# Performance work log

Measured on AMD Instinct MI355X. Metric: run time of the kernel, lower is better.

Reference implementation:

```python
import jax, jax.numpy as jnp
import numpy as np


def setup_inputs() -> dict:
    key = jax.random.key(0)
    k1, k2, k3, k4 = jax.random.split(key, 4)
    B, S, E, H = 8, 2048, 1024, 64
    x = jax.random.normal(k1, (B, S, E), dtype=jnp.float32)
    scale = 1.0 / np.sqrt(E)
    Wq = jax.random.normal(k2, (E, H), dtype=jnp.float32) * scale
    Wk = jax.random.normal(k3, (E, H), dtype=jnp.float32) * scale
    Wv = jax.random.normal(k4, (E, H), dtype=jnp.float32) * scale
    return {"x": x, "Wq": Wq, "Wk": Wk, "Wv": Wv}


def reference(x, Wq, Wk, Wv):
    # x: [B, S, E]; Wq/Wk/Wv: [E, H]
    B, S, E = x.shape
    H = Wq.shape[1]
    q = x @ Wq  # [B, S, H]
    k = x @ Wk
    v = x @ Wv
    inv_sqrt_h = 1.0 / jnp.sqrt(jnp.asarray(H, dtype=x.dtype))
    att = jnp.einsum("bqh,bkh->bqk", q, k) * inv_sqrt_h  # [B, S, S]
    causal = jnp.tril(jnp.ones((S, S), dtype=bool))
    att = jnp.where(causal, att, jnp.asarray(-jnp.inf, dtype=att.dtype))
    att = jax.nn.softmax(att, axis=-1)
    # dropout p=0.0 (eval) -> identity
    return jnp.einsum("bqk,bkh->bqh", att, v)  # [B, S, H]
```

## Files before the change

### kernel.cpp

```cpp
#include <hip/hip_runtime.h>
#include <math.h>

typedef __attribute__((ext_vector_type(8))) short bf16x8;
typedef __attribute__((ext_vector_type(16))) float fx16;

#define SEQ 2048
#define HD 64

__device__ __forceinline__ unsigned f2bf_bits(float f){
  unsigned u = __float_as_uint(f);
  return (u + 0x7fffu + ((u >> 16) & 1u)) >> 16;
}
__device__ __forceinline__ unsigned cvt_pk_bf16(float a, float b){
  unsigned r;
  asm("v_cvt_pk_bf16_f32 %0, %1, %2" : "=v"(r) : "v"(a), "v"(b));
  return r;
}
__device__ __forceinline__ float lo16f(unsigned u){ return __uint_as_float(u << 16); }
__device__ __forceinline__ float hi16f(unsigned u){ return __uint_as_float(u & 0xffff0000u); }
union U8 { bf16x8 v; short s[8]; unsigned u[4]; };

__device__ __forceinline__ fx16 mfma_bf16(bf16x8 a, bf16x8 b, fx16 c){
  return __builtin_amdgcn_mfma_f32_32x32x16_bf16(a, b, c, 0, 0, 0);
}
__device__ __forceinline__ fx16 fzero(){
  fx16 z;
#pragma unroll
  for (int i = 0; i < 16; ++i) z[i] = 0.f;
  return z;
}

__global__ __launch_bounds__(256) void wconv_kernel(
    const float* __restrict__ Wq, const float* __restrict__ Wk, const float* __restrict__ Wv,
    short* __restrict__ wsB)
{
  int gid = blockIdx.x * 4 + (threadIdx.x >> 6);
  int lane = threadIdx.x & 63;
  int l31 = lane & 31, h = lane >> 5;
  int half = gid & 1;
  int rem = gid >> 1;
  int t = rem % 6;
  int stage = rem / 6;
  int n = t * 32 + l31;
  int mat = n >> 6, col = n & 63;
  const float* W = (mat == 0) ? Wq : (mat == 1) ? Wk : Wv;
  int kbase = stage * 16 + h * 8;
  U8 o;
#pragma unroll
  for (int i = 0; i < 8; ++i) {
    float f = W[(size_t)(kbase + i) * 64 + col];
    unsigned hb = f2bf_bits(f);
    if (half == 0) o.s[i] = (short)hb;
    else {
      float hf = __uint_as_float(hb << 16);
      o.s[i] = (short)f2bf_bits(f - hf);
    }
  }
  *(bf16x8*)(wsB + (size_t)gid * 512 + lane * 8) = o.v;
}

__global__ __launch_bounds__(512) void proj_kernel(
    const float* __restrict__ x, const short* __restrict__ wsB,
    short* __restrict__ qh, short* __restrict__ ql,
    short* __restrict__ kh, short* __restrict__ kl,
    short* __restrict__ vth, short* __restrict__ vtl)
{
  __shared__ float Rx[4][3 * 16 * 64];
  __shared__ float Vb[32 * 68];

  const int tid = threadIdx.x;
  const int lane = tid & 63, w = tid >> 6;
  const int l31 = lane & 31, h = lane >> 5;
  const int ksel = w >> 1;
  const int nsel = w & 1;
  const int row0 = blockIdx.x * 32;
  const size_t xbase = (size_t)(row0 + l31) * 1024;

  fx16 acc[3];
#pragma unroll
  for (int t = 0; t < 3; ++t) acc[t] = fzero();

#pragma unroll 4
  for (int s = 0; s < 16; ++s) {
    const int stage = ksel * 16 + s;
    const int k = stage * 16 + h * 8;
    float4 fa = *(const float4*)(x + xbase + k);
    float4 fb = *(const float4*)(x + xbase + k + 4);
    U8 ah, al;
    ah.u[0] = cvt_pk_bf16(fa.x, fa.y);
    ah.u[1] = cvt_pk_bf16(fa.z, fa.w);
    ah.u[2] = cvt_pk_bf16(fb.x, fb.y);
    ah.u[3] = cvt_pk_bf16(fb.z, fb.w);
    al.u[0] = cvt_pk_bf16(fa.x - lo16f(ah.u[0]), fa.y - hi16f(ah.u[0]));
    al.u[1] = cvt_pk_bf16(fa.z - lo16f(ah.u[1]), fa.w - hi16f(ah.u[1]));
    al.u[2] = cvt_pk_bf16(fb.x - lo16f(ah.u[2]), fb.y - hi16f(ah.u[2]));
    al.u[3] = cvt_pk_bf16(fb.z - lo16f(ah.u[3]), fb.w - hi16f(ah.u[3]));
#pragma unroll
    for (int tt = 0; tt < 3; ++tt) {
      const int tg = nsel * 3 + tt;
      const size_t g2 = ((size_t)stage * 6 + tg) * 2;
      bf16x8 Bh = *(const bf16x8*)(wsB + g2 * 512 + lane * 8);
      bf16x8 Bl = *(const bf16x8*)(wsB + g2 * 512 + 512 + lane * 8);
      acc[tt] = mfma_bf16(al.v, Bh, acc[tt]);
      acc[tt] = mfma_bf16(ah.v, Bl, acc[tt]);
      acc[tt] = mfma_bf16(ah.v, Bh, acc[tt]);
    }
  }

  if (ksel == 1 || ksel == 3) {
    const int ws_ = (ksel == 1) ? nsel : 2 + nsel;
#pragma unroll
    for (int t = 0; t < 3; ++t)
#pragma unroll
      for (int r = 0; r < 16; ++r)
        Rx[ws_][t * 1024 + r * 64 + lane] = acc[t][r];
  }
  __syncthreads();
  if (ksel == 0 || ksel == 2) {
    const int rs_ = (ksel == 0) ? nsel : 2 + nsel;
#pragma unroll
    for (int t = 0; t < 3; ++t)
#pragma unroll
      for (int r = 0; r < 16; ++r)
        acc[t][r] += Rx[rs_][t * 1024 + r * 64 + lane];
  }
  __syncthreads();
  if (ksel == 2) {
#pragma unroll
    for (int t = 0; t < 3; ++t)
#pragma unroll
      for (int r = 0; r < 16; ++r)
        Rx[nsel][t * 1024 + r * 64 + lane] = acc[t][r];
  }
  __syncthreads();
  if (ksel == 0) {
#pragma unroll
    for (int t = 0; t < 3; ++t) {
      const int tg = nsel * 3 + t;
      const int mat = tg >> 1;
      const int colb = (tg & 1) * 32 + l31;
#pragma unroll
      for (int r = 0; r < 16; ++r)
        acc[t][r] += Rx[nsel][t * 1024 + r * 64 + lane];
      if (mat < 2) {
        short* dh = (mat == 0) ? qh : kh;
        short* dl = (mat == 0) ? ql : kl;
#pragma unroll
        for (int r = 0; r < 16; ++r) {
          float f = acc[t][r];
          int rowg = row0 + (r & 3) + 8 * (r >> 2) + 4 * h;
          unsigned hb = f2bf_bits(f);
          float hf = __uint_as_float(hb << 16);
          unsigned lb = f2bf_bits(f - hf);
          dh[(size_t)rowg * 64 + colb] = (short)hb;
          dl[(size_t)rowg * 64 + colb] = (short)lb;
        }
      } else {
#pragma unroll
        for (int r = 0; r < 16; ++r) {
          float f = acc[t][r];
          int srel = (r & 3) + 8 * (r >> 2) + 4 * h;
          Vb[srel * 68 + (tg - 4) * 32 + l31] = f;
        }
      }
    }
  }
  __syncthreads();
  if (tid < 256) {
    int d = tid >> 2, s8 = (tid & 3) * 8;
    int bb = row0 >> 11, s0 = row0 & 2047;
    U8 hv, lv;
#pragma unroll
    for (int ss = 0; ss < 8; ++ss) {
      float f = Vb[(s8 + ss) * 68 + d];
      unsigned hb = f2bf_bits(f);
      float hf = __uint_as_float(hb << 16);
      hv.s[ss] = (short)hb;
      lv.s[ss] = (short)f2bf_bits(f - hf);
    }
    size_t o = (size_t)(bb * 64 + d) * 2048 + s0 + s8;
    *(bf16x8*)(vth + o) = hv.v;
    *(bf16x8*)(vtl + o) = lv.v;
  }
}

__global__ __launch_bounds__(64) void attn_kernel(
    const short* __restrict__ qh, const short* __restrict__ ql,
    const short* __restrict__ kh, const short* __restrict__ kl,
    const short* __restrict__ vth, const short* __restrict__ vtl,
    float* __restrict__ segO, float* __restrict__ segL, float* __restrict__ segM)
{
  const int bid = blockIdx.x;
  const int b = bid & 7;
  int r = bid >> 3;
  int qt = 0, acc = 0;
  while (r >= acc + ((qt + 5) / 5)) { acc += (qt + 5) / 5; ++qt; }
  const int sg = r - acc;
  const int nk = qt + 1;
  const int kt0 = sg * 5;
  int nsteps = nk - kt0; if (nsteps > 5) nsteps = 5;

  const int lane = threadIdx.x;
  const int l31 = lane & 31, h = lane >> 5;
  const int qabs = qt * 32 + l31;

  bf16x8 qf0[4], qf1[4];
  {
    size_t qrow = ((size_t)b * 2048 + qabs) * 64;
#pragma unroll
    for (int ds = 0; ds < 4; ++ds) {
      qf0[ds] = *(const bf16x8*)(qh + qrow + ds * 16 + 8 * h);
      qf1[ds] = *(const bf16x8*)(ql + qrow + ds * 16 + 8 * h);
    }
  }

  fx16 acc0 = fzero(), acc1 = fzero();
  float Mrun = -3e38f, lrun = 0.f;

  for (int it = 0; it < nsteps; ++it) {
    const int kt = kt0 + it;
    bf16x8 kah[4], kal[4];
    {
      const size_t koff = ((size_t)b * 2048 + (size_t)kt * 32 + l31) * 64 + 8 * h;
#pragma unroll
      for (int ds = 0; ds < 4; ++ds) {
        kah[ds] = *(const bf16x8*)(kh + koff + ds * 16);
        kal[ds] = *(const bf16x8*)(kl + koff + ds * 16);
      }
    }
    bf16x8 vfh[2][2], vfl[2][2];
#pragma unroll
    for (int kp = 0; kp < 2; ++kp)
#pragma unroll
      for (int md = 0; md < 2; ++md) {
        const size_t vrow = (size_t)(b * 64 + md * 32 + l31) * 2048 + kt * 32 + kp * 16 + 8 * h;
        vfh[kp][md] = *(const bf16x8*)(vth + vrow);
        vfl[kp][md] = *(const bf16x8*)(vtl + vrow);
      }

    fx16 stA = fzero(), stB = fzero();
    __builtin_amdgcn_s_setprio(1);
#pragma unroll
    for (int ds = 0; ds < 4; ++ds) {
      stA = mfma_bf16(kah[ds], qf0[ds], stA);
      stB = mfma_bf16(kal[ds], qf0[ds], stB);
      stB = mfma_bf16(kah[ds], qf1[ds], stB);
    }
    __builtin_amdgcn_s_setprio(0);

    float sv[16];
    const bool diag = (kt == qt);
#pragma unroll
    for (int r2 = 0; r2 < 16; ++r2) {
      float s = (stA[r2] + stB[r2]) * 0.125f;
      if (diag) {
        int ka = kt * 32 + (r2 & 3) + 8 * (r2 >> 2) + 4 * h;
        if (ka > qabs) s = -3e38f;
      }
      sv[r2] = s;
    }
    float tm = sv[0];
#pragma unroll
    for (int r2 = 1; r2 < 16; ++r2) tm = fmaxf(tm, sv[r2]);
    tm = fmaxf(tm, __shfl_xor(tm, 32, 64));
    float Mnew = fmaxf(Mrun, tm);
    float alpha = __expf(Mrun - Mnew);
    Mrun = Mnew;
    float psum = 0.f;
#pragma unroll
    for (int r2 = 0; r2 < 16; ++r2) { sv[r2] = __expf(sv[r2] - Mnew); psum += sv[r2]; }
    psum += __shfl_xor(psum, 32, 64);
    lrun = lrun * alpha + psum;
#pragma unroll
    for (int r2 = 0; r2 < 16; ++r2) { acc0[r2] *= alpha; acc1[r2] *= alpha; }

    unsigned chv[8], clv[8];
#pragma unroll
    for (int q2 = 0; q2 < 8; ++q2) {
      unsigned c = cvt_pk_bf16(sv[2 * q2], sv[2 * q2 + 1]);
      chv[q2] = c;
      clv[q2] = cvt_pk_bf16(sv[2 * q2] - lo16f(c), sv[2 * q2 + 1] - hi16f(c));
    }
#pragma unroll
    for (int kp = 0; kp < 2; ++kp) {
      U8 ph, pl;
      {
        unsigned c0 = chv[4 * kp], c1 = chv[4 * kp + 1], c2 = chv[4 * kp + 2], c3 = chv[4 * kp + 3];
        unsigned x0 = (unsigned)__shfl_xor((int)c0, 32, 64);
        unsigned x1 = (unsigned)__shfl_xor((int)c1, 32, 64);
        unsigned x2 = (unsigned)__shfl_xor((int)c2, 32, 64);
        unsigned x3 = (unsigned)__shfl_xor((int)c3, 32, 64);
        ph.u[0] = h ? x2 : c0;  ph.u[1] = h ? x3 : c1;
        ph.u[2] = h ? c2 : x0;  ph.u[3] = h ? c3 : x1;
        c0 = clv[4 * kp]; c1 = clv[4 * kp + 1]; c2 = clv[4 * kp + 2]; c3 = clv[4 * kp + 3];
        x0 = (unsigned)__shfl_xor((int)c0, 32, 64);
        x1 = (unsigned)__shfl_xor((int)c1, 32, 64);
        x2 = (unsigned)__shfl_xor((int)c2, 32, 64);
        x3 = (unsigned)__shfl_xor((int)c3, 32, 64);
        pl.u[0] = h ? x2 : c0;  pl.u[1] = h ? x3 : c1;
        pl.u[2] = h ? c2 : x0;  pl.u[3] = h ? c3 : x1;
      }
      __builtin_amdgcn_s_setprio(1);
      acc0 = mfma_bf16(vfl[kp][0], ph.v, acc0);
      acc0 = mfma_bf16(vfh[kp][0], pl.v, acc0);
      acc0 = mfma_bf16(vfh[kp][0], ph.v, acc0);
      acc1 = mfma_bf16(vfl[kp][1], ph.v, acc1);
      acc1 = mfma_bf16(vfh[kp][1], pl.v, acc1);
      acc1 = mfma_bf16(vfh[kp][1], ph.v, acc1);
      __builtin_amdgcn_s_setprio(0);
    }
  }

  float* o = segO + (size_t)bid * 2048;
#pragma unroll
  for (int md = 0; md < 2; ++md) {
#pragma unroll
    for (int r2 = 0; r2 < 16; ++r2) {
      int d = md * 32 + (r2 & 3) + 8 * (r2 >> 2) + 4 * h;
      float val = md ? acc1[r2] : acc0[r2];
      o[d * 32 + l31] = val;
    }
  }
  if (h == 0) {
    segL[(size_t)bid * 32 + l31] = lrun;
    segM[(size_t)bid * 32 + l31] = Mrun;
  }
}

__global__ __launch_bounds__(256) void combine_kernel(
    const float* __restrict__ segO, const float* __restrict__ segL,
    const float* __restrict__ segM, float* __restrict__ out)
{
  __shared__ float Sc[13][32];
  __shared__ float Linv[32];
  __shared__ float Ot[64 * 40];

  const int bq = blockIdx.x;
  const int b = bq >> 6, qt = bq & 63;
  const int nsg = (qt + 5) / 5;
  int base = 0;
  for (int i = 0; i < qt; ++i) base += (i + 5) / 5;
  const int tid = threadIdx.x;

  if (tid < 32) {
    float M = -3e38f;
    for (int s = 0; s < nsg; ++s)
      M = fmaxf(M, segM[(size_t)((base + s) * 8 + b) * 32 + tid]);
    float L = 0.f;
    for (int s = 0; s < nsg; ++s) {
      float e = __expf(segM[(size_t)((base + s) * 8 + b) * 32 + tid] - M);
      Sc[s][tid] = e;
      L += e * segL[(size_t)((base + s) * 8 + b) * 32 + tid];
    }
    Linv[tid] = 1.f / L;
  }
  __syncthreads();
  {
#pragma unroll
    for (int i = tid; i < 512; i += 256) {
      int d = i >> 3, q4 = (i & 7) * 4;
      float4 a = {0.f, 0.f, 0.f, 0.f};
      for (int s = 0; s < nsg; ++s) {
        float4 v = *(const float4*)(segO + (size_t)((base + s) * 8 + b) * 2048 + d * 32 + q4);
        a.x += Sc[s][q4 + 0] * v.x;
        a.y += Sc[s][q4 + 1] * v.y;
        a.z += Sc[s][q4 + 2] * v.z;
        a.w += Sc[s][q4 + 3] * v.w;
      }
      *(float4*)&Ot[d * 40 + q4] = a;
    }
  }
  __syncthreads();
  {
    const int q = tid >> 3, dc = (tid & 7) * 8;
    const float inv = Linv[q];
    float* dst = out + ((size_t)b * 2048 + qt * 32 + q) * 64 + dc;
#pragma unroll
    for (int i = 0; i < 2; ++i) {
      float4 o;
      o.x = Ot[(dc + 4 * i + 0) * 40 + q] * inv;
      o.y = Ot[(dc + 4 * i + 1) * 40 + q] * inv;
      o.z = Ot[(dc + 4 * i + 2) * 40 + q] * inv;
      o.w = Ot[(dc + 4 * i + 3) * 40 + q] * inv;
      *(float4*)(dst + 4 * i) = o;
    }
  }
}

extern "C" void kernel_launch(void* const* d_in, const int* in_sizes, int n_in,
                              void* d_out, int out_size, void* d_ws, size_t ws_size,
                              hipStream_t stream) {
  const float* x  = (const float*)d_in[0];
  const float* Wq = (const float*)d_in[1];
  const float* Wk = (const float*)d_in[2];
  const float* Wv = (const float*)d_in[3];

  char* wsb = (char*)d_ws;
  short* wsB = (short*)(wsb + 0);
  short* qh  = (short*)(wsb + 786432);
  short* ql  = (short*)(wsb + 2883584);
  short* kh  = (short*)(wsb + 4980736);
  short* kl  = (short*)(wsb + 7077888);
  short* vth = (short*)(wsb + 9175040);
  short* vtl = (short*)(wsb + 11272192);
  float* segO = (float*)(wsb + 13369344);
  float* segL = (float*)(wsb + 42336256);
  float* segM = (float*)(wsb + 42788864);

  wconv_kernel<<<192, 256, 0, stream>>>(Wq, Wk, Wv, wsB);
  proj_kernel<<<512, 512, 0, stream>>>(x, wsB, qh, ql, kh, kl, vth, vtl);
  attn_kernel<<<3536, 64, 0, stream>>>(qh, ql, kh, kl, vth, vtl, segO, segL, segM);
  combine_kernel<<<512, 256, 0, stream>>>(segO, segL, segM, (float*)d_out);
}
```

Measured before the change: 102.9 us.

## Double row tiles in projection and attention to reuse weight and K/V fragments

The projection kernel now handles 64 rows per block instead of 32, so each weight fragment load feeds two MFMA row tiles. The cross-wave K-split reduction becomes a serial accumulate into a smaller shared buffer. The attention kernel processes two 32-row query groups per wave, sharing each loaded K/V tile between them, and the segment and combine layouts change to match. This halves global loads of weights and K/V per unit of work, at the cost of higher register pressure, fewer blocks (less parallelism), and more serial reduction barriers in projection.

```diff
diff --git a/kernel.cpp b/kernel.cpp
--- a/kernel.cpp
+++ b/kernel.cpp
@@ -65,122 +65,235 @@
     short* __restrict__ kh, short* __restrict__ kl,
     short* __restrict__ vth, short* __restrict__ vtl)
 {
-  __shared__ float Rx[4][3 * 16 * 64];
-  __shared__ float Vb[32 * 68];
+  __shared__ float Rx[2][6144];
 
   const int tid = threadIdx.x;
   const int lane = tid & 63, w = tid >> 6;
   const int l31 = lane & 31, h = lane >> 5;
   const int ksel = w >> 1;
   const int nsel = w & 1;
-  const int row0 = blockIdx.x * 32;
-  const size_t xbase = (size_t)(row0 + l31) * 1024;
-
-  fx16 acc[3];
-#pragma unroll
-  for (int t = 0; t < 3; ++t) acc[t] = fzero();
-
-#pragma unroll 4
+  const int row0 = blockIdx.x * 64;
+  const size_t xb0 = (size_t)(row0 + l31) * 1024;
+  const size_t xb1 = (size_t)(row0 + 32 + l31) * 1024;
+
+  fx16 a0[3], a1[3];
+#pragma unroll
+  for (int t = 0; t < 3; ++t) { a0[t] = fzero(); a1[t] = fzero(); }
+
+#pragma unroll 2
   for (int s = 0; s < 16; ++s) {
     const int stage = ksel * 16 + s;
     const int k = stage * 16 + h * 8;
-    float4 fa = *(const float4*)(x + xbase + k);
-    float4 fb = *(const float4*)(x + xbase + k + 4);
-    U8 ah, al;
-    ah.u[0] = cvt_pk_bf16(fa.x, fa.y);
-    ah.u[1] = cvt_pk_bf16(fa.z, fa.w);
-    ah.u[2] = cvt_pk_bf16(fb.x, fb.y);
-    ah.u[3] = cvt_pk_bf16(fb.z, fb.w);
-    al.u[0] = cvt_pk_bf16(fa.x - lo16f(ah.u[0]), fa.y - hi16f(ah.u[0]));
-    al.u[1] = cvt_pk_bf16(fa.z - lo16f(ah.u[1]), fa.w - hi16f(ah.u[1]));
-    al.u[2] = cvt_pk_bf16(fb.x - lo16f(ah.u[2]), fb.y - hi16f(ah.u[2]));
-    al.u[3] = cvt_pk_bf16(fb.z - lo16f(ah.u[3]), fb.w - hi16f(ah.u[3]));
+    float4 fa0 = *(const float4*)(x + xb0 + k);
+    float4 fb0 = *(const float4*)(x + xb0 + k + 4);
+    float4 fa1 = *(const float4*)(x + xb1 + k);
+    float4 fb1 = *(const float4*)(x + xb1 + k + 4);
+    U8 ah0, al0, ah1, al1;
+    ah0.u[0] = cvt_pk_bf16(fa0.x, fa0.y);
+    ah0.u[1] = cvt_pk_bf16(fa0.z, fa0.w);
+    ah0.u[2] = cvt_pk_bf16(fb0.x, fb0.y);
+    ah0.u[3] = cvt_pk_bf16(fb0.z, fb0.w);
+    al0.u[0] = cvt_pk_bf16(fa0.x - lo16f(ah0.u[0]), fa0.y - hi16f(ah0.u[0]));
+    al0.u[1] = cvt_pk_bf16(fa0.z - lo16f(ah0.u[1]), fa0.w - hi16f(ah0.u[1]));
+    al0.u[2] = cvt_pk_bf16(fb0.x - lo16f(ah0.u[2]), fb0.y - hi16f(ah0.u[2]));
+    al0.u[3] = cvt_pk_bf16(fb0.z - lo16f(ah0.u[3]), fb0.w - hi16f(ah0.u[3]));
+    ah1.u[0] = cvt_pk_bf16(fa1.x, fa1.y);
+    ah1.u[1] = cvt_pk_bf16(fa1.z, fa1.w);
+    ah1.u[2] = cvt_pk_bf16(fb1.x, fb1.y);
+    ah1.u[3] = cvt_pk_bf16(fb1.z, fb1.w);
+    al1.u[0] = cvt_pk_bf16(fa1.x - lo16f(ah1.u[0]), fa1.y - hi16f(ah1.u[0]));
+    al1.u[1] = cvt_pk_bf16(fa1.z - lo16f(ah1.u[1]), fa1.w - hi16f(ah1.u[1]));
+    al1.u[2] = cvt_pk_bf16(fb1.x - lo16f(ah1.u[2]), fb1.y - hi16f(ah1.u[2]));
+    al1.u[3] = cvt_pk_bf16(fb1.z - lo16f(ah1.u[3]), fb1.w - hi16f(ah1.u[3]));
 #pragma unroll
     for (int tt = 0; tt < 3; ++tt) {
       const int tg = nsel * 3 + tt;
       const size_t g2 = ((size_t)stage * 6 + tg) * 2;
       bf16x8 Bh = *(const bf16x8*)(wsB + g2 * 512 + lane * 8);
       bf16x8 Bl = *(const bf16x8*)(wsB + g2 * 512 + 512 + lane * 8);
-      acc[tt] = mfma_bf16(al.v, Bh, acc[tt]);
-      acc[tt] = mfma_bf16(ah.v, Bl, acc[tt]);
-      acc[tt] = mfma_bf16(ah.v, Bh, acc[tt]);
-    }
-  }
-
-  if (ksel == 1 || ksel == 3) {
-    const int ws_ = (ksel == 1) ? nsel : 2 + nsel;
-#pragma unroll
-    for (int t = 0; t < 3; ++t)
-#pragma unroll
-      for (int r = 0; r < 16; ++r)
-        Rx[ws_][t * 1024 + r * 64 + lane] = acc[t][r];
-  }
-  __syncthreads();
-  if (ksel == 0 || ksel == 2) {
-    const int rs_ = (ksel == 0) ? nsel : 2 + nsel;
-#pragma unroll
-    for (int t = 0; t < 3; ++t)
-#pragma unroll
-      for (int r = 0; r < 16; ++r)
-        acc[t][r] += Rx[rs_][t * 1024 + r * 64 + lane];
+      a0[tt] = mfma_bf16(al0.v, Bh, a0[tt]);
+      a0[tt] = mfma_bf16(ah0.v, Bl, a0[tt]);
+      a0[tt] = mfma_bf16(ah0.v, Bh, a0[tt]);
+      a1[tt] = mfma_bf16(al1.v, Bh, a1[tt]);
+      a1[tt] = mfma_bf16(ah1.v, Bl, a1[tt]);
+      a1[tt] = mfma_bf16(ah1.v, Bh, a1[tt]);
+    }
+  }
+
+  float* slot = &Rx[nsel][0];
+  __syncthreads();
+  if (ksel == 3) {
+#pragma unroll
+    for (int tt = 0; tt < 3; ++tt)
+#pragma unroll
+      for (int r = 0; r < 16; ++r) {
+        slot[((tt * 2 + 0) * 16 + r) * 64 + lane] = a0[tt][r];
+        slot[((tt * 2 + 1) * 16 + r) * 64 + lane] = a1[tt][r];
+      }
   }
   __syncthreads();
   if (ksel == 2) {
 #pragma unroll
-    for (int t = 0; t < 3; ++t)
-#pragma unroll
-      for (int r = 0; r < 16; ++r)
-        Rx[nsel][t * 1024 + r * 64 + lane] = acc[t][r];
+    for (int tt = 0; tt < 3; ++tt)
+#pragma unroll
+      for (int r = 0; r < 16; ++r) {
+        slot[((tt * 2 + 0) * 16 + r) * 64 + lane] += a0[tt][r];
+        slot[((tt * 2 + 1) * 16 + r) * 64 + lane] += a1[tt][r];
+      }
+  }
+  __syncthreads();
+  if (ksel == 1) {
+#pragma unroll
+    for (int tt = 0; tt < 3; ++tt)
+#pragma unroll
+      for (int r = 0; r < 16; ++r) {
+        slot[((tt * 2 + 0) * 16 + r) * 64 + lane] += a0[tt][r];
+        slot[((tt * 2 + 1) * 16 + r) * 64 + lane] += a1[tt][r];
+      }
   }
   __syncthreads();
   if (ksel == 0) {
 #pragma unroll
-    for (int t = 0; t < 3; ++t) {
-      const int tg = nsel * 3 + t;
+    for (int tt = 0; tt < 3; ++tt)
+#pragma unroll
+      for (int r = 0; r < 16; ++r) {
+        a0[tt][r] += slot[((tt * 2 + 0) * 16 + r) * 64 + lane];
+        a1[tt][r] += slot[((tt * 2 + 1) * 16 + r) * 64 + lane];
+      }
+  }
+  __syncthreads();
+
+  float* Vb = &Rx[0][0];
+  if (ksel == 0) {
+#pragma unroll
+    for (int tt = 0; tt < 3; ++tt) {
+      const int tg = nsel * 3 + tt;
       const int mat = tg >> 1;
       const int colb = (tg & 1) * 32 + l31;
-#pragma unroll
-      for (int r = 0; r < 16; ++r)
-        acc[t][r] += Rx[nsel][t * 1024 + r * 64 + lane];
       if (mat < 2) {
         short* dh = (mat == 0) ? qh : kh;
         short* dl = (mat == 0) ? ql : kl;
 #pragma unroll
-        for (int r = 0; r < 16; ++r) {
-          float f = acc[t][r];
-          int rowg = row0 + (r & 3) + 8 * (r >> 2) + 4 * h;
-          unsigned hb = f2bf_bits(f);
-          float hf = __uint_as_float(hb << 16);
-          unsigned lb = f2bf_bits(f - hf);
-          dh[(size_t)rowg * 64 + colb] = (short)hb;
-          dl[(size_t)rowg * 64 + colb] = (short)lb;
-        }
+        for (int m = 0; m < 2; ++m)
+#pragma unroll
+          for (int r = 0; r < 16; ++r) {
+            float f = (m ? a1[tt][r] : a0[tt][r]);
+            int rowg = row0 + m * 32 + (r & 3) + 8 * (r >> 2) + 4 * h;
+            unsigned hb = f2bf_bits(f);
+            float hf = __uint_as_float(hb << 16);
+            unsigned lb = f2bf_bits(f - hf);
+            dh[(size_t)rowg * 64 + colb] = (short)hb;
+            dl[(size_t)rowg * 64 + colb] = (short)lb;
+          }
       } else {
 #pragma unroll
-        for (int r = 0; r < 16; ++r) {
-          float f = acc[t][r];
-          int srel = (r & 3) + 8 * (r >> 2) + 4 * h;
-          Vb[srel * 68 + (tg - 4) * 32 + l31] = f;
-        }
+        for (int m = 0; m < 2; ++m)
+#pragma unroll
+          for (int r = 0; r < 16; ++r) {
+            float f = (m ? a1[tt][r] : a0[tt][r]);
+            int srel = m * 32 + (r & 3) + 8 * (r >> 2) + 4 * h;
+            Vb[srel * 68 + (tg - 4) * 32 + l31] = f;
+          }
       }
     }
   }
   __syncthreads();
   if (tid < 256) {
-    int d = tid >> 2, s8 = (tid & 3) * 8;
+    int d = tid >> 2, sc = (tid & 3) * 16;
     int bb = row0 >> 11, s0 = row0 & 2047;
-    U8 hv, lv;
-#pragma unroll
-    for (int ss = 0; ss < 8; ++ss) {
-      float f = Vb[(s8 + ss) * 68 + d];
+    U8 hv0, hv1, lv0, lv1;
+#pragma unroll
+    for (int ss = 0; ss < 16; ++ss) {
+      float f = Vb[(sc + ss) * 68 + d];
       unsigned hb = f2bf_bits(f);
       float hf = __uint_as_float(hb << 16);
-      hv.s[ss] = (short)hb;
-      lv.s[ss] = (short)f2bf_bits(f - hf);
-    }
-    size_t o = (size_t)(bb * 64 + d) * 2048 + s0 + s8;
-    *(bf16x8*)(vth + o) = hv.v;
-    *(bf16x8*)(vtl + o) = lv.v;
+      unsigned lb = f2bf_bits(f - hf);
+      if (ss < 8) { hv0.s[ss] = (short)hb; lv0.s[ss] = (short)lb; }
+      else        { hv1.s[ss - 8] = (short)hb; lv1.s[ss - 8] = (short)lb; }
+    }
+    size_t o = (size_t)(bb * 64 + d) * 2048 + s0 + sc;
+    *(bf16x8*)(vth + o) = hv0.v;  *(bf16x8*)(vth + o + 8) = hv1.v;
+    *(bf16x8*)(vtl + o) = lv0.v;  *(bf16x8*)(vtl + o + 8) = lv1.v;
+  }
+}
+
+__device__ __forceinline__ void attn_step_qg(
+    const bf16x8* __restrict__ qh_, const bf16x8* __restrict__ ql_,
+    const bf16x8* __restrict__ kah, const bf16x8* __restrict__ kal,
+    const bf16x8 (*vfh)[2], const bf16x8 (*vfl)[2],
+    fx16& accA, fx16& accB, float& Mrun, float& lrun,
+    const int kt, const int qt, const int qg, const int h, const int qabs)
+{
+  fx16 st = fzero();
+  __builtin_amdgcn_s_setprio(1);
+#pragma unroll
+  for (int ds = 0; ds < 4; ++ds) {
+    st = mfma_bf16(kah[ds], qh_[ds], st);
+    st = mfma_bf16(kal[ds], qh_[ds], st);
+    st = mfma_bf16(kah[ds], ql_[ds], st);
+  }
+  __builtin_amdgcn_s_setprio(0);
+
+  float sv[16];
+  const bool diag = (kt == 2 * qt + qg);
+#pragma unroll
+  for (int r2 = 0; r2 < 16; ++r2) {
+    float s = st[r2] * 0.125f;
+    if (diag) {
+      int ka = kt * 32 + (r2 & 3) + 8 * (r2 >> 2) + 4 * h;
+      if (ka > qabs) s = -3e38f;
+    }
+    sv[r2] = s;
+  }
+  float tm = sv[0];
+#pragma unroll
+  for (int r2 = 1; r2 < 16; ++r2) tm = fmaxf(tm, sv[r2]);
+  tm = fmaxf(tm, __shfl_xor(tm, 32, 64));
+  float Mnew = fmaxf(Mrun, tm);
+  float alpha = __expf(Mrun - Mnew);
+  Mrun = Mnew;
+  float psum = 0.f;
+#pragma unroll
+  for (int r2 = 0; r2 < 16; ++r2) { sv[r2] = __expf(sv[r2] - Mnew); psum += sv[r2]; }
+  psum += __shfl_xor(psum, 32, 64);
+  lrun = lrun * alpha + psum;
+#pragma unroll
+  for (int r2 = 0; r2 < 16; ++r2) { accA[r2] *= alpha; accB[r2] *= alpha; }
+
+  unsigned chv[8], clv[8];
+#pragma unroll
+  for (int q2 = 0; q2 < 8; ++q2) {
+    unsigned c = cvt_pk_bf16(sv[2 * q2], sv[2 * q2 + 1]);
+    chv[q2] = c;
+    clv[q2] = cvt_pk_bf16(sv[2 * q2] - lo16f(c), sv[2 * q2 + 1] - hi16f(c));
+  }
+#pragma unroll
+  for (int kp = 0; kp < 2; ++kp) {
+    U8 ph, pl;
+    {
+      unsigned c0 = chv[4 * kp], c1 = chv[4 * kp + 1], c2 = chv[4 * kp + 2], c3 = chv[4 * kp + 3];
+      unsigned x0 = (unsigned)__shfl_xor((int)c0, 32, 64);
+      unsigned x1 = (unsigned)__shfl_xor((int)c1, 32, 64);
+      unsigned x2 = (unsigned)__shfl_xor((int)c2, 32, 64);
+      unsigned x3 = (unsigned)__shfl_xor((int)c3, 32, 64);
+      ph.u[0] = h ? x2 : c0;  ph.u[1] = h ? x3 : c1;
+      ph.u[2] = h ? c2 : x0;  ph.u[3] = h ? c3 : x1;
+      c0 = clv[4 * kp]; c1 = clv[4 * kp + 1]; c2 = clv[4 * kp + 2]; c3 = clv[4 * kp + 3];
+      x0 = (unsigned)__shfl_xor((int)c0, 32, 64);
+      x1 = (unsigned)__shfl_xor((int)c1, 32, 64);
+      x2 = (unsigned)__shfl_xor((int)c2, 32, 64);
+      x3 = (unsigned)__shfl_xor((int)c3, 32, 64);
+      pl.u[0] = h ? x2 : c0;  pl.u[1] = h ? x3 : c1;
+      pl.u[2] = h ? c2 : x0;  pl.u[3] = h ? c3 : x1;
+    }
+    __builtin_amdgcn_s_setprio(1);
+    accA = mfma_bf16(vfl[kp][0], ph.v, accA);
+    accA = mfma_bf16(vfh[kp][0], pl.v, accA);
+    accA = mfma_bf16(vfh[kp][0], ph.v, accA);
+    accB = mfma_bf16(vfl[kp][1], ph.v, accB);
+    accB = mfma_bf16(vfh[kp][1], pl.v, accB);
+    accB = mfma_bf16(vfh[kp][1], ph.v, accB);
+    __builtin_amdgcn_s_setprio(0);
   }
 }
 
@@ -194,28 +307,32 @@
   const int b = bid & 7;
   int r = bid >> 3;
   int qt = 0, acc = 0;
-  while (r >= acc + ((qt + 5) / 5)) { acc += (qt + 5) / 5; ++qt; }
+  while (r >= acc + ((2 * qt + 6) / 5)) { acc += (2 * qt + 6) / 5; ++qt; }
   const int sg = r - acc;
-  const int nk = qt + 1;
+  const int nk = 2 * qt + 2;
   const int kt0 = sg * 5;
   int nsteps = nk - kt0; if (nsteps > 5) nsteps = 5;
 
   const int lane = threadIdx.x;
   const int l31 = lane & 31, h = lane >> 5;
-  const int qabs = qt * 32 + l31;
-
-  bf16x8 qf0[4], qf1[4];
+  const int qa0 = qt * 64 + l31;
+  const int qa1 = qt * 64 + 32 + l31;
+
+  bf16x8 q0h[4], q0l[4], q1h[4], q1l[4];
   {
-    size_t qrow = ((size_t)b * 2048 + qabs) * 64;
+    size_t r0 = ((size_t)b * 2048 + qt * 64 + l31) * 64 + 8 * h;
+    size_t r1 = r0 + 32 * 64;
 #pragma unroll
     for (int ds = 0; ds < 4; ++ds) {
-      qf0[ds] = *(const bf16x8*)(qh + qrow + ds * 16 + 8 * h);
-      qf1[ds] = *(const bf16x8*)(ql + qrow + ds * 16 + 8 * h);
-    }
-  }
-
-  fx16 acc0 = fzero(), acc1 = fzero();
-  float Mrun = -3e38f, lrun = 0.f;
+      q0h[ds] = *(const bf16x8*)(qh + r0 + ds * 16);
+      q0l[ds] = *(const bf16x8*)(ql + r0 + ds * 16);
+      q1h[ds] = *(const bf16x8*)(qh + r1 + ds * 16);
+      q1l[ds] = *(const bf16x8*)(ql + r1 + ds * 16);
+    }
+  }
+
+  fx16 a00 = fzero(), a01 = fzero(), a10 = fzero(), a11 = fzero();
+  float M0 = -3e38f, L0 = 0.f, M1 = -3e38f, L1 = 0.f;
 
   for (int it = 0; it < nsteps; ++it) {
     const int kt = kt0 + it;
@@ -238,92 +355,25 @@
         vfl[kp][md] = *(const bf16x8*)(vtl + vrow);
       }
 
-    fx16 stA = fzero(), stB = fzero();
-    __builtin_amdgcn_s_setprio(1);
-#pragma unroll
-    for (int ds = 0; ds < 4; ++ds) {
-      stA = mfma_bf16(kah[ds], qf0[ds], stA);
-      stB = mfma_bf16(kal[ds], qf0[ds], stB);
-      stB = mfma_bf16(kah[ds], qf1[ds], stB);
-    }
-    __builtin_amdgcn_s_setprio(0);
-
-    float sv[16];
-    const bool diag = (kt == qt);
-#pragma unroll
-    for (int r2 = 0; r2 < 16; ++r2) {
-      float s = (stA[r2] + stB[r2]) * 0.125f;
-      if (diag) {
-        int ka = kt * 32 + (r2 & 3) + 8 * (r2 >> 2) + 4 * h;
-        if (ka > qabs) s = -3e38f;
-      }
-      sv[r2] = s;
-    }
-    float tm = sv[0];
-#pragma unroll
-    for (int r2 = 1; r2 < 16; ++r2) tm = fmaxf(tm, sv[r2]);
-    tm = fmaxf(tm, __shfl_xor(tm, 32, 64));
-    float Mnew = fmaxf(Mrun, tm);
-    float alpha = __expf(Mrun - Mnew);
-    Mrun = Mnew;
-    float psum = 0.f;
-#pragma unroll
-    for (int r2 = 0; r2 < 16; ++r2) { sv[r2] = __expf(sv[r2] - Mnew); psum += sv[r2]; }
-    psum += __shfl_xor(psum, 32, 64);
-    lrun = lrun * alpha + psum;
-#pragma unroll
-    for (int r2 = 0; r2 < 16; ++r2) { acc0[r2] *= alpha; acc1[r2] *= alpha; }
-
-    unsigned chv[8], clv[8];
-#pragma unroll
-    for (int q2 = 0; q2 < 8; ++q2) {
-      unsigned c = cvt_pk_bf16(sv[2 * q2], sv[2 * q2 + 1]);
-      chv[q2] = c;
-      clv[q2] = cvt_pk_bf16(sv[2 * q2] - lo16f(c), sv[2 * q2 + 1] - hi16f(c));
-    }
-#pragma unroll
-    for (int kp = 0; kp < 2; ++kp) {
-      U8 ph, pl;
-      {
-        unsigned c0 = chv[4 * kp], c1 = chv[4 * kp + 1], c2 = chv[4 * kp + 2], c3 = chv[4 * kp + 3];
-        unsigned x0 = (unsigned)__shfl_xor((int)c0, 32, 64);
-        unsigned x1 = (unsigned)__shfl_xor((int)c1, 32, 64);
-        unsigned x2 = (unsigned)__shfl_xor((int)c2, 32, 64);
-        unsigned x3 = (unsigned)__shfl_xor((int)c3, 32, 64);
-        ph.u[0] = h ? x2 : c0;  ph.u[1] = h ? x3 : c1;
-        ph.u[2] = h ? c2 : x0;  ph.u[3] = h ? c3 : x1;
-        c0 = clv[4 * kp]; c1 = clv[4 * kp + 1]; c2 = clv[4 * kp + 2]; c3 = clv[4 * kp + 3];
-        x0 = (unsigned)__shfl_xor((int)c0, 32, 64);
-        x1 = (unsigned)__shfl_xor((int)c1, 32, 64);
-        x2 = (unsigned)__shfl_xor((int)c2, 32, 64);
-        x3 = (unsigned)__shfl_xor((int)c3, 32, 64);
-        pl.u[0] = h ? x2 : c0;  pl.u[1] = h ? x3 : c1;
-        pl.u[2] = h ? c2 : x0;  pl.u[3] = h ? c3 : x1;
-      }
-      __builtin_amdgcn_s_setprio(1);
-      acc0 = mfma_bf16(vfl[kp][0], ph.v, acc0);
-      acc0 = mfma_bf16(vfh[kp][0], pl.v, acc0);
-      acc0 = mfma_bf16(vfh[kp][0], ph.v, acc0);
-      acc1 = mfma_bf16(vfl[kp][1], ph.v, acc1);
-      acc1 = mfma_bf16(vfh[kp][1], pl.v, acc1);
-      acc1 = mfma_bf16(vfh[kp][1], ph.v, acc1);
-      __builtin_amdgcn_s_setprio(0);
-    }
-  }
-
-  float* o = segO + (size_t)bid * 2048;
-#pragma unroll
-  for (int md = 0; md < 2; ++md) {
-#pragma unroll
-    for (int r2 = 0; r2 < 16; ++r2) {
-      int d = md * 32 + (r2 & 3) + 8 * (r2 >> 2) + 4 * h;
-      float val = md ? acc1[r2] : acc0[r2];
-      o[d * 32 + l31] = val;
-    }
+    if (kt <= 2 * qt)
+      attn_step_qg(q0h, q0l, kah, kal, vfh, vfl, a00, a01, M0, L0, kt, qt, 0, h, qa0);
+    attn_step_qg(q1h, q1l, kah, kal, vfh, vfl, a10, a11, M1, L1, kt, qt, 1, h, qa1);
+  }
+
+  float* o = segO + (size_t)bid * 4096;
+#pragma unroll
+  for (int r2 = 0; r2 < 16; ++r2) {
+    int d0 = (r2 & 3) + 8 * (r2 >> 2) + 4 * h;
+    o[d0 * 64 + l31]             = a00[r2];
+    o[(32 + d0) * 64 + l31]      = a01[r2];
+    o[d0 * 64 + 32 + l31]        = a10[r2];
+    o[(32 + d0) * 64 + 32 + l31] = a11[r2];
   }
   if (h == 0) {
-    segL[(size_t)bid * 32 + l31] = lrun;
-    segM[(size_t)bid * 32 + l31] = Mrun;
+    segL[(size_t)bid * 64 + l31]      = L0;
+    segL[(size_t)bid * 64 + 32 + l31] = L1;
+    segM[(size_t)bid * 64 + l31]      = M0;
+    segM[(size_t)bid * 64 + 32 + l31] = M1;
   }
 }
 
@@ -331,57 +381,56 @@
     const float* __restrict__ segO, const float* __restrict__ segL,
     const float* __restrict__ segM, float* __restrict__ out)
 {
-  __shared__ float Sc[13][32];
-  __shared__ float Linv[32];
-  __shared__ float Ot[64 * 40];
+  __shared__ float Sc[13][64];
+  __shared__ float Linv[64];
+  __shared__ float Ot[64 * 68];
 
   const int bq = blockIdx.x;
-  const int b = bq >> 6, qt = bq & 63;
-  const int nsg = (qt + 5) / 5;
+  const int b = bq >> 5, qt = bq & 31;
+  const int nsg = (2 * qt + 6) / 5;
   int base = 0;
-  for (int i = 0; i < qt; ++i) base += (i + 5) / 5;
+  for (int i = 0; i < qt; ++i) base += (2 * i + 6) / 5;
   const int tid = threadIdx.x;
 
-  if (tid < 32) {
+  if (tid < 64) {
     float M = -3e38f;
     for (int s = 0; s < nsg; ++s)
-      M = fmaxf(M, segM[(size_t)((base + s) * 8 + b) * 32 + tid]);
+      M = fmaxf(M, segM[(size_t)((base + s) * 8 + b) * 64 + tid]);
     float L = 0.f;
     for (int s = 0; s < nsg; ++s) {
-      float e = __expf(segM[(size_t)((base + s) * 8 + b) * 32 + tid] - M);
+      float e = __expf(segM[(size_t)((base + s) * 8 + b) * 64 + tid] - M);
       Sc[s][tid] = e;
-      L += e * segL[(size_t)((base + s) * 8 + b) * 32 + tid];
+      L += e * segL[(size_t)((base + s) * 8 + b) * 64 + tid];
     }
     Linv[tid] = 1.f / L;
   }
   __syncthreads();
   {
-#pragma unroll
-    for (int i = tid; i < 512; i += 256) {
-      int d = i >> 3, q4 = (i & 7) * 4;
+    for (int i = tid; i < 1024; i += 256) {
+      int d = i >> 4, q4 = (i & 15) * 4;
       float4 a = {0.f, 0.f, 0.f, 0.f};
       for (int s = 0; s < nsg; ++s) {
-        float4 v = *(const float4*)(segO + (size_t)((base + s) * 8 + b) * 2048 + d * 32 + q4);
+        float4 v = *(const float4*)(segO + (size_t)((base + s) * 8 + b) * 4096 + d * 64 + q4);
         a.x += Sc[s][q4 + 0] * v.x;
         a.y += Sc[s][q4 + 1] * v.y;
         a.z += Sc[s][q4 + 2] * v.z;
         a.w += Sc[s][q4 + 3] * v.w;
       }
-      *(float4*)&Ot[d * 40 + q4] = a;
+      *(float4*)&Ot[d * 68 + q4] = a;
     }
   }
   __syncthreads();
   {
-    const int q = tid >> 3, dc = (tid & 7) * 8;
+    const int q = tid >> 2, dc = (tid & 3) * 16;
     const float inv = Linv[q];
-    float* dst = out + ((size_t)b * 2048 + qt * 32 + q) * 64 + dc;
-#pragma unroll
-    for (int i = 0; i < 2; ++i) {
+    float* dst = out + ((size_t)b * 2048 + qt * 64 + q) * 64 + dc;
+#pragma unroll
+    for (int i = 0; i < 4; ++i) {
       float4 o;
-      o.x = Ot[(dc + 4 * i + 0) * 40 + q] * inv;
-      o.y = Ot[(dc + 4 * i + 1) * 40 + q] * inv;
-      o.z = Ot[(dc + 4 * i + 2) * 40 + q] * inv;
-      o.w = Ot[(dc + 4 * i + 3) * 40 + q] * inv;
+      o.x = Ot[(dc + 4 * i + 0) * 68 + q] * inv;
+      o.y = Ot[(dc + 4 * i + 1) * 68 + q] * inv;
+      o.z = Ot[(dc + 4 * i + 2) * 68 + q] * inv;
+      o.w = Ot[(dc + 4 * i + 3) * 68 + q] * inv;
       *(float4*)(dst + 4 * i) = o;
     }
   }
@@ -404,11 +453,11 @@
   short* vth = (short*)(wsb + 9175040);
   short* vtl = (short*)(wsb + 11272192);
   float* segO = (float*)(wsb + 13369344);
-  float* segL = (float*)(wsb + 42336256);
-  float* segM = (float*)(wsb + 42788864);
+  float* segL = (float*)(wsb + 42729472);
+  float* segM = (float*)(wsb + 43188224);
 
   wconv_kernel<<<192, 256, 0, stream>>>(Wq, Wk, Wv, wsB);
-  proj_kernel<<<512, 512, 0, stream>>>(x, wsB, qh, ql, kh, kl, vth, vtl);
-  attn_kernel<<<3536, 64, 0, stream>>>(qh, ql, kh, kl, vth, vtl, segO, segL, segM);
-  combine_kernel<<<512, 256, 0, stream>>>(segO, segL, segM, (float*)d_out);
-}
+  proj_kernel<<<256, 512, 0, stream>>>(x, wsB, qh, ql, kh, kl, vth, vtl);
+  attn_kernel<<<1792, 64, 0, stream>>>(qh, ql, kh, kl, vth, vtl, segO, segL, segM);
+  combine_kernel<<<256, 256, 0, stream>>>(segO, segL, segM, (float*)d_out);
+}
```

New measurement: 112.1 us. 8.9% more time.

## Rebalance causal key-split segments by query group and prefetch next K tile

Applied to the files above, without the earlier changes.

Query tiles are now grouped in eights, and each group of g gets g+1 key segments whose lengths are balanced. This replaces fixed five-tile segments and cuts the attention grid from 3536 to 2304 blocks, so the combine kernel has fewer partials to merge and less partial output to write. The K tile for the next step is loaded one iteration ahead so its latency overlaps the current step's MFMA work. In exchange, segments grow to up to about eight tiles, which lengthens the critical path and raises register pressure from the extra prefetch registers.

```diff
diff --git a/kernel.cpp b/kernel.cpp
--- a/kernel.cpp
+++ b/kernel.cpp
@@ -192,13 +192,17 @@
 {
   const int bid = blockIdx.x;
   const int b = bid & 7;
-  int r = bid >> 3;
-  int qt = 0, acc = 0;
-  while (r >= acc + ((qt + 5) / 5)) { acc += (qt + 5) / 5; ++qt; }
-  const int sg = r - acc;
+  const int r = bid >> 3;
+  int g = 0;
+  while (r >= 4 * (g + 1) * (g + 2)) ++g;
+  const int rr = r - 4 * g * (g + 1);
+  const int qt = g * 8 + rr / (g + 1);
+  const int sg = rr % (g + 1);
   const int nk = qt + 1;
-  const int kt0 = sg * 5;
-  int nsteps = nk - kt0; if (nsteps > 5) nsteps = 5;
+  const int nsg = g + 1;
+  const int bs = nk / nsg, rem = nk % nsg;
+  const int nsteps = bs + (sg < rem ? 1 : 0);
+  const int kt0 = sg * bs + (sg < rem ? sg : rem);
 
   const int lane = threadIdx.x;
   const int l31 = lane & 31, h = lane >> 5;
@@ -217,17 +221,18 @@
   fx16 acc0 = fzero(), acc1 = fzero();
   float Mrun = -3e38f, lrun = 0.f;
 
+  bf16x8 kah[4], kal[4];
+  {
+    const size_t koff = ((size_t)b * 2048 + (size_t)kt0 * 32 + l31) * 64 + 8 * h;
+#pragma unroll
+    for (int ds = 0; ds < 4; ++ds) {
+      kah[ds] = *(const bf16x8*)(kh + koff + ds * 16);
+      kal[ds] = *(const bf16x8*)(kl + koff + ds * 16);
+    }
+  }
+
   for (int it = 0; it < nsteps; ++it) {
     const int kt = kt0 + it;
-    bf16x8 kah[4], kal[4];
-    {
-      const size_t koff = ((size_t)b * 2048 + (size_t)kt * 32 + l31) * 64 + 8 * h;
-#pragma unroll
-      for (int ds = 0; ds < 4; ++ds) {
-        kah[ds] = *(const bf16x8*)(kh + koff + ds * 16);
-        kal[ds] = *(const bf16x8*)(kl + koff + ds * 16);
-      }
-    }
     bf16x8 vfh[2][2], vfl[2][2];
 #pragma unroll
     for (int kp = 0; kp < 2; ++kp)
@@ -237,6 +242,16 @@
         vfh[kp][md] = *(const bf16x8*)(vth + vrow);
         vfl[kp][md] = *(const bf16x8*)(vtl + vrow);
       }
+    const int kn = (it + 1 < nsteps) ? kt + 1 : kt;
+    bf16x8 knh[4], knl[4];
+    {
+      const size_t koff = ((size_t)b * 2048 + (size_t)kn * 32 + l31) * 64 + 8 * h;
+#pragma unroll
+      for (int ds = 0; ds < 4; ++ds) {
+        knh[ds] = *(const bf16x8*)(kh + koff + ds * 16);
+        knl[ds] = *(const bf16x8*)(kl + koff + ds * 16);
+      }
+    }
 
     fx16 stA = fzero(), stB = fzero();
     __builtin_amdgcn_s_setprio(1);
@@ -309,6 +324,8 @@
       acc1 = mfma_bf16(vfh[kp][1], ph.v, acc1);
       __builtin_amdgcn_s_setprio(0);
     }
+#pragma unroll
+    for (int ds = 0; ds < 4; ++ds) { kah[ds] = knh[ds]; kal[ds] = knl[ds]; }
   }
 
   float* o = segO + (size_t)bid * 2048;
@@ -331,15 +348,14 @@
     const float* __restrict__ segO, const float* __restrict__ segL,
     const float* __restrict__ segM, float* __restrict__ out)
 {
-  __shared__ float Sc[13][32];
+  __shared__ float Sc[8][32];
   __shared__ float Linv[32];
   __shared__ float Ot[64 * 40];
 
   const int bq = blockIdx.x;
   const int b = bq >> 6, qt = bq & 63;
-  const int nsg = (qt + 5) / 5;
-  int base = 0;
-  for (int i = 0; i < qt; ++i) base += (i + 5) / 5;
+  const int g = qt >> 3, nsg = g + 1;
+  const int base = 4 * g * (g + 1) + (qt & 7) * nsg;
   const int tid = threadIdx.x;
 
   if (tid < 32) {
@@ -404,11 +420,11 @@
   short* vth = (short*)(wsb + 9175040);
   short* vtl = (short*)(wsb + 11272192);
   float* segO = (float*)(wsb + 13369344);
-  float* segL = (float*)(wsb + 42336256);
-  float* segM = (float*)(wsb + 42788864);
+  float* segL = (float*)(wsb + 32243712);
+  float* segM = (float*)(wsb + 32538624);
 
   wconv_kernel<<<192, 256, 0, stream>>>(Wq, Wk, Wv, wsB);
   proj_kernel<<<512, 512, 0, stream>>>(x, wsB, qh, ql, kh, kl, vth, vtl);
-  attn_kernel<<<3536, 64, 0, stream>>>(qh, ql, kh, kl, vth, vtl, segO, segL, segM);
+  attn_kernel<<<2304, 64, 0, stream>>>(qh, ql, kh, kl, vth, vtl, segO, segL, segM);
   combine_kernel<<<512, 256, 0, stream>>>(segO, segL, segM, (float*)d_out);
 }
```

Result: faster. 99.53 us (-3.3%).
